# Kernel optimization log

Measured on AMD Instinct MI355X. Metric: run time of the kernel, lower is better.

## Reference

```python
import jax, jax.numpy as jnp
import numpy as np
import math

NUM_HEADS = 32
NUM_KV = 8
D = 128          # num_hidden == per-head dim in this module
S = 2048
B = 1
DK = 128
ROPE_BASE = 10000.0


def rope(x):
    # x: [B, H, S, D]; standard Llama-style RoPE (split-halves rotation) over positions.
    d = x.shape[-1]
    half = d // 2
    pos = jnp.arange(x.shape[2], dtype=jnp.float32)                       # [S]
    inv_freq = 1.0 / (ROPE_BASE ** (jnp.arange(half, dtype=jnp.float32) / half))
    ang = pos[:, None] * inv_freq[None, :]                                # [S, half]
    cos = jnp.cos(ang)
    sin = jnp.sin(ang)
    x1 = x[..., :half]
    x2 = x[..., half:]
    return jnp.concatenate([x1 * cos - x2 * sin, x1 * sin + x2 * cos], axis=-1)


def setup_inputs() -> dict:
    key = jax.random.key(0)
    ks = jax.random.split(key, 8)
    query = jax.random.normal(ks[0], (B, S, D), dtype=jnp.float32)
    k_in = jax.random.normal(ks[1], (B, S, D), dtype=jnp.float32)
    v_in = jax.random.normal(ks[2], (B, S, D), dtype=jnp.float32)
    # causal mask: 1 where attention allowed (lower triangle incl diagonal)
    mask = jnp.tril(jnp.ones((S, S), dtype=jnp.int32))[None, None]        # [1,1,S,S]
    sc = 0.02
    Wq = jax.random.normal(ks[3], (NUM_HEADS * D, D), dtype=jnp.float32) * sc
    bq = jnp.zeros((NUM_HEADS * D,), dtype=jnp.float32)
    Wk = jax.random.normal(ks[4], (NUM_KV * D, D), dtype=jnp.float32) * sc
    bk = jnp.zeros((NUM_KV * D,), dtype=jnp.float32)
    Wv = jax.random.normal(ks[5], (NUM_KV * D, D), dtype=jnp.float32) * sc
    bv = jnp.zeros((NUM_KV * D,), dtype=jnp.float32)
    Wo = jax.random.normal(ks[6], (D, NUM_HEADS * D), dtype=jnp.float32) * sc
    bo = jnp.zeros((D,), dtype=jnp.float32)
    return {"query": query, "key": k_in, "values": v_in, "mask": mask,
            "Wq": Wq, "bq": bq, "Wk": Wk, "bk": bk, "Wv": Wv, "bv": bv,
            "Wo": Wo, "bo": bo}


def reference(query, key, values, mask, Wq, bq, Wk, bk, Wv, bv, Wo, bo):
    Bq, Sq, Dh = query.shape
    # projections; torch Linear: x @ W.T + b. Note: view (reshape), not transpose,
    # exactly as in the original module.
    q = (query @ Wq.T + bq).reshape(Bq, NUM_HEADS, Sq, Dh)   # [B,H,S,D]
    k = (key @ Wk.T + bk).reshape(Bq, NUM_KV, Sq, Dh)        # [B,Hkv,S,D]
    v = (values @ Wv.T + bv).reshape(Bq, NUM_KV, Sq, Dh)
    rk = rope(k)
    rv = rope(v)  # module applies RoPE to values too (faithful)
    rep = NUM_HEADS // NUM_KV
    # torch .repeat((1, rep, 1, 1)) tiles whole head blocks -> jnp.tile
    rk = jnp.tile(rk, (1, rep, 1, 1))                        # [B,H,S,D]
    rv = jnp.tile(rv, (1, rep, 1, 1))
    scores = jnp.einsum('bhqd,bhkd->bhqk', q, rk) / math.sqrt(DK)
    scores = jnp.where(mask == 0, -jnp.inf, scores)
    attn = jax.nn.softmax(scores, axis=-1)
    out = jnp.einsum('bhqk,bhkd->bhqd', attn, rv)            # [B,H,S,D]
    out = out.transpose(0, 2, 1, 3).reshape(Bq, Sq, NUM_HEADS * Dh)
    return out @ Wo.T + bo
```

## Files before the change

### kernel.cpp

```cpp
#include <hip/hip_runtime.h>

typedef unsigned short u16;
typedef unsigned int u32;
typedef short frag_t __attribute__((ext_vector_type(8)));
typedef float f32x4 __attribute__((ext_vector_type(4)));

#define S_LEN 2048

__device__ __forceinline__ float bf2f(u32 u) {
  union { u32 i; float f; } v; v.i = u << 16; return v.f;
}
__device__ __forceinline__ u16 f2bf(float f) {
  u32 x = __float_as_uint(f);
  u32 r = (x + 0x7fffu + ((x >> 16) & 1u)) >> 16;
  return (u16)r;
}
__device__ __forceinline__ void unpack8(uint4 r, float* o) {
  o[0] = bf2f(r.x & 0xffffu); o[1] = bf2f(r.x >> 16);
  o[2] = bf2f(r.y & 0xffffu); o[3] = bf2f(r.y >> 16);
  o[4] = bf2f(r.z & 0xffffu); o[5] = bf2f(r.z >> 16);
  o[6] = bf2f(r.w & 0xffffu); o[7] = bf2f(r.w >> 16);
}
__device__ __forceinline__ u16 ld_in(const void* p, size_t idx, bool fp32) {
  if (fp32) return f2bf(((const float*)p)[idx]);
  return ((const u16*)p)[idx];
}
__device__ __forceinline__ uint4 ld8(const void* p, size_t eidx, bool fp32) {
  if (!fp32) return *(const uint4*)((const u16*)p + eidx);
  const float4* f = (const float4*)((const float*)p + eidx);
  float4 x = f[0], y = f[1];
  uint4 r;
  r.x = (u32)f2bf(x.x) | ((u32)f2bf(x.y) << 16);
  r.y = (u32)f2bf(x.z) | ((u32)f2bf(x.w) << 16);
  r.z = (u32)f2bf(y.x) | ((u32)f2bf(y.y) << 16);
  r.w = (u32)f2bf(y.z) | ((u32)f2bf(y.w) << 16);
  return r;
}

__global__ void detect_dtype(const u16* __restrict__ q, u32* __restrict__ flag) {
  int t = threadIdx.x;
  u32 e = ((u32)q[2 * t] >> 7) & 0xFFu;
  bool ok = (e >= 110u && e <= 140u);
  unsigned long long b = __ballot(ok);
  if (t == 0) *flag = (__popcll(b) < 32) ? 1u : 0u;
}

__global__ __launch_bounds__(256) void proj_all(
    const void* __restrict__ query, const void* __restrict__ key,
    const void* __restrict__ values,
    const void* __restrict__ Wq, const void* __restrict__ bq,
    const void* __restrict__ Wk, const void* __restrict__ bk,
    const void* __restrict__ Wv, const void* __restrict__ bv,
    u16* __restrict__ Qb, u16* __restrict__ Kb, u16* __restrict__ Vtmp,
    const u32* __restrict__ flagp) {
  __shared__ u16 As[64][136];
  __shared__ u16 Ws[64][136];
  const bool fp32 = (*flagp != 0u);
  const int t = threadIdx.x;
  const int x = blockIdx.x;
  const void *A, *W, *bias;
  u16* C; int N, n0;
  if (x < 64)      { A = query;  W = Wq; bias = bq; C = Qb;   N = 4096; n0 = x << 6; }
  else if (x < 80) { A = key;    W = Wk; bias = bk; C = Kb;   N = 1024; n0 = (x - 64) << 6; }
  else             { A = values; W = Wv; bias = bv; C = Vtmp; N = 1024; n0 = (x - 80) << 6; }
  const int m0 = blockIdx.y << 6;
  for (int i = t; i < 1024; i += 256) {
    int r = i >> 4, d8 = (i & 15) << 3;
    *(uint4*)&As[r][d8] = ld8(A, (size_t)(m0 + r) * 128 + d8, fp32);
    *(uint4*)&Ws[r][d8] = ld8(W, (size_t)(n0 + r) * 128 + d8, fp32);
  }
  __syncthreads();
  const int lane = t & 63, w = t >> 6, quad = lane >> 4, l15 = lane & 15;
  f32x4 acc[4];
#pragma unroll
  for (int nt = 0; nt < 4; ++nt) acc[nt] = 0.f;
#pragma unroll
  for (int kc = 0; kc < 4; ++kc) {
    frag_t a = *(const frag_t*)&As[w * 16 + l15][kc * 32 + quad * 8];
#pragma unroll
    for (int nt = 0; nt < 4; ++nt) {
      frag_t b = *(const frag_t*)&Ws[nt * 16 + l15][kc * 32 + quad * 8];
      acc[nt] = __builtin_amdgcn_mfma_f32_16x16x32_bf16(a, b, acc[nt], 0, 0, 0);
    }
  }
#pragma unroll
  for (int nt = 0; nt < 4; ++nt) {
    int n = n0 + nt * 16 + l15;
    float bb = bf2f((u32)ld_in(bias, n, fp32));
#pragma unroll
    for (int r = 0; r < 4; ++r) {
      int m = m0 + w * 16 + quad * 4 + r;
      C[(size_t)m * N + n] = f2bf(acc[nt][r] + bb);
    }
  }
}

__global__ __launch_bounds__(256) void rope_kv_tr(u16* __restrict__ Kb,
                                                  const u16* __restrict__ Vb,
                                                  u16* __restrict__ VbT) {
  __shared__ u16 Lt[128][72];
  const int t = threadIdx.x;
  const int s0 = blockIdx.x << 6;
  const int g = blockIdx.y;
  for (int i = t; i < 4096; i += 256) {
    int s = s0 + (i >> 6), ii = i & 63;
    float invf = __expf(-(float)ii * 0.14391156831212787f);
    float ang = (float)s * invf;
    float sn, cs;
    sincosf(ang, &sn, &cs);
    size_t base = ((size_t)(g << 11) + s) * 128 + ii;
    float k1 = bf2f((u32)Kb[base]), k2 = bf2f((u32)Kb[base + 64]);
    Kb[base] = f2bf(k1 * cs - k2 * sn);
    Kb[base + 64] = f2bf(k1 * sn + k2 * cs);
  }
  const u16* src = Vb + (size_t)g * S_LEN * 128;
  for (int i = t; i < 512; i += 256) {
    int r = i >> 3, d8 = (i & 7) << 3;
    float lo[8], hi[8];
    unpack8(*(const uint4*)&src[(size_t)(s0 + r) * 128 + d8], lo);
    unpack8(*(const uint4*)&src[(size_t)(s0 + r) * 128 + d8 + 64], hi);
#pragma unroll
    for (int j = 0; j < 8; ++j) {
      float invf = __expf(-(float)(d8 + j) * 0.14391156831212787f);
      float ang = (float)(s0 + r) * invf;
      float sn, cs;
      sincosf(ang, &sn, &cs);
      Lt[d8 + j][r] = f2bf(lo[j] * cs - hi[j] * sn);
      Lt[d8 + 64 + j][r] = f2bf(lo[j] * sn + hi[j] * cs);
    }
  }
  __syncthreads();
  u16* dst = VbT + (size_t)g * 128 * S_LEN + s0;
  for (int i = t; i < 2048; i += 256) {
    int d = i >> 4, s4 = (i & 15) << 2;
    uint2 pk;
    pk.x = (u32)Lt[d][s4] | ((u32)Lt[d][s4 + 1] << 16);
    pk.y = (u32)Lt[d][s4 + 2] | ((u32)Lt[d][s4 + 3] << 16);
    *(uint2*)&dst[(size_t)d * S_LEN + s4] = pk;
  }
}

__global__ __launch_bounds__(512, 2) void attn_mfma(
    const u16* __restrict__ Qb, const u16* __restrict__ Kb,
    const u16* __restrict__ VbT, u16* __restrict__ Ob) {
  __shared__ __align__(16) char smem[106496];
  u16 (*Kt)[136] = (u16(*)[136])smem;
  u16 (*Vt)[136] = (u16(*)[136])(smem + 34816);
  u16 (*St)[72]  = (u16(*)[72]) (smem + 69632);
  float* Om = (float*)smem;
  float* Ml = (float*)(smem + 65536);
  const int t = threadIdx.x;
  const int lane = t & 63, w = t >> 6, quad = lane >> 4, l15 = lane & 15;
  const int hw = w & 3, half = w >> 2;
  const int g = blockIdx.y;
  const int pi = blockIdx.x;
  const int h = g + (hw << 3);
  const u16* Kg = Kb + (size_t)g * S_LEN * 128;
  const u16* Vg = VbT + (size_t)g * 128 * S_LEN;
  const int srow = t >> 4, scol = (t & 15) << 3;

  for (int tp = 0; tp < 2; ++tp) {
    const int qt = tp ? pi : 63 - pi;
    const int q0 = qt << 5;
    frag_t aq[2][4];
#pragma unroll
    for (int qp = 0; qp < 2; ++qp)
#pragma unroll
      for (int kc = 0; kc < 4; ++kc)
        aq[qp][kc] = *(const frag_t*)&Qb[((size_t)h * S_LEN + q0 + qp * 16 + l15) * 128 +
                                         kc * 32 + quad * 8];
    float m_r[2] = {-1e30f, -1e30f}, l_r[2] = {0.f, 0.f};
    f32x4 oacc[2][8];
#pragma unroll
    for (int qp = 0; qp < 2; ++qp)
#pragma unroll
      for (int nt = 0; nt < 8; ++nt) oacc[qp][nt] = 0.f;
    const int niter64 = (qt >> 1) + 1;
    const int niter2 = (niter64 + 1) >> 1;

    uint4 kpf[4], vpf[4];
#pragma unroll
    for (int j = 0; j < 4; ++j) {
      kpf[j] = *(const uint4*)&Kg[(size_t)(srow + j * 32) * 128 + scol];
      vpf[j] = *(const uint4*)&Vg[(size_t)(srow + j * 32) * S_LEN + scol];
    }

    for (int kt2 = 0; kt2 < niter2; ++kt2) {
      __syncthreads();
#pragma unroll
      for (int j = 0; j < 4; ++j) {
        *(uint4*)&Kt[srow + j * 32][scol] = kpf[j];
        *(uint4*)&Vt[srow + j * 32][scol] = vpf[j];
      }
      __syncthreads();
      if (kt2 + 1 < niter2) {
        const int kn = (kt2 + 1) << 7;
#pragma unroll
        for (int j = 0; j < 4; ++j) {
          kpf[j] = *(const uint4*)&Kg[(size_t)(kn + srow + j * 32) * 128 + scol];
          vpf[j] = *(const uint4*)&Vg[(size_t)(srow + j * 32) * S_LEN + kn + scol];
        }
      }
      const int tile64 = (kt2 << 1) + half;
      if (tile64 < niter64) {
        const int lk = half << 6;
        const int kbase = (kt2 << 7) + lk;
        f32x4 s4[4][2];
#pragma unroll
        for (int kk = 0; kk < 4; ++kk)
#pragma unroll
          for (int qp = 0; qp < 2; ++qp) s4[kk][qp] = 0.f;
#pragma unroll
        for (int kc = 0; kc < 4; ++kc) {
#pragma unroll
          for (int kk = 0; kk < 4; ++kk) {
            frag_t a = *(const frag_t*)&Kt[lk + kk * 16 + l15][kc * 32 + quad * 8];
            s4[kk][0] = __builtin_amdgcn_mfma_f32_16x16x32_bf16(a, aq[0][kc], s4[kk][0], 0, 0, 0);
            s4[kk][1] = __builtin_amdgcn_mfma_f32_16x16x32_bf16(a, aq[1][kc], s4[kk][1], 0, 0, 0);
          }
        }
        const bool lastm = (tile64 == niter64 - 1);
        float alpha[2];
#pragma unroll
        for (int qp = 0; qp < 2; ++qp) {
          const int qg = q0 + qp * 16 + l15;
          float mx = -1e30f;
#pragma unroll
          for (int kk = 0; kk < 4; ++kk)
#pragma unroll
            for (int r = 0; r < 4; ++r) {
              float sv = s4[kk][qp][r] * 0.08838834764831845f;
              if (lastm && (kbase + kk * 16 + quad * 4 + r) > qg) sv = -1e30f;
              s4[kk][qp][r] = sv;
              mx = fmaxf(mx, sv);
            }
          mx = fmaxf(mx, __shfl_xor(mx, 16));
          mx = fmaxf(mx, __shfl_xor(mx, 32));
          float mn = fmaxf(m_r[qp], mx);
          alpha[qp] = __expf(m_r[qp] - mn);
          m_r[qp] = mn;
          float sum = 0.f;
          const int strow = w * 32 + qp * 16 + l15;
#pragma unroll
          for (int kk = 0; kk < 4; ++kk) {
            float p0 = __expf(s4[kk][qp][0] - mn);
            float p1 = __expf(s4[kk][qp][1] - mn);
            float p2 = __expf(s4[kk][qp][2] - mn);
            float p3 = __expf(s4[kk][qp][3] - mn);
            sum += (p0 + p1) + (p2 + p3);
            uint2 pk;
            pk.x = (u32)f2bf(p0) | ((u32)f2bf(p1) << 16);
            pk.y = (u32)f2bf(p2) | ((u32)f2bf(p3) << 16);
            *(uint2*)&St[strow][kk * 16 + quad * 4] = pk;
          }
          sum += __shfl_xor(sum, 16);
          sum += __shfl_xor(sum, 32);
          l_r[qp] = l_r[qp] * alpha[qp] + sum;
        }
#pragma unroll
        for (int qp = 0; qp < 2; ++qp)
#pragma unroll
          for (int r = 0; r < 4; ++r) {
            float al = __shfl(alpha[qp], quad * 4 + r);
#pragma unroll
            for (int nt = 0; nt < 8; ++nt) oacc[qp][nt][r] *= al;
          }
#pragma unroll
        for (int kc2 = 0; kc2 < 2; ++kc2) {
          frag_t pa[2];
#pragma unroll
          for (int qp = 0; qp < 2; ++qp)
            pa[qp] = *(const frag_t*)&St[w * 32 + qp * 16 + l15][kc2 * 32 + quad * 8];
#pragma unroll
          for (int nt = 0; nt < 8; ++nt) {
            frag_t v = *(const frag_t*)&Vt[nt * 16 + l15][lk + kc2 * 32 + quad * 8];
            oacc[0][nt] = __builtin_amdgcn_mfma_f32_16x16x32_bf16(pa[0], v, oacc[0][nt], 0, 0, 0);
            oacc[1][nt] = __builtin_amdgcn_mfma_f32_16x16x32_bf16(pa[1], v, oacc[1][nt], 0, 0, 0);
          }
        }
      }
    }
    __syncthreads();
    if (half == 1) {
#pragma unroll
      for (int qp = 0; qp < 2; ++qp)
#pragma unroll
        for (int nt = 0; nt < 8; ++nt)
#pragma unroll
          for (int r = 0; r < 4; ++r)
            Om[((hw * 32) + qp * 16 + quad * 4 + r) * 128 + nt * 16 + l15] = oacc[qp][nt][r];
      if (quad == 0) {
#pragma unroll
        for (int qp = 0; qp < 2; ++qp) {
          Ml[hw * 64 + qp * 16 + l15] = m_r[qp];
          Ml[hw * 64 + 32 + qp * 16 + l15] = l_r[qp];
        }
      }
    }
    __syncthreads();
    if (half == 0) {
      float v1[2], v2[2];
#pragma unroll
      for (int qp = 0; qp < 2; ++qp) {
        float m2 = Ml[hw * 64 + qp * 16 + l15];
        float l2 = Ml[hw * 64 + 32 + qp * 16 + l15];
        float mn = fmaxf(m_r[qp], m2);
        float a1 = __expf(m_r[qp] - mn);
        float a2 = __expf(m2 - mn);
        float linv = 1.0f / (a1 * l_r[qp] + a2 * l2);
        v1[qp] = a1 * linv;
        v2[qp] = a2 * linv;
      }
#pragma unroll
      for (int qp = 0; qp < 2; ++qp)
#pragma unroll
        for (int r = 0; r < 4; ++r) {
          float w1 = __shfl(v1[qp], quad * 4 + r);
          float w2 = __shfl(v2[qp], quad * 4 + r);
          int q = q0 + qp * 16 + quad * 4 + r;
#pragma unroll
          for (int nt = 0; nt < 8; ++nt) {
            float o2 = Om[((hw * 32) + qp * 16 + quad * 4 + r) * 128 + nt * 16 + l15];
            Ob[(size_t)q * 4096 + h * 128 + nt * 16 + l15] =
                f2bf(oacc[qp][nt][r] * w1 + o2 * w2);
          }
        }
    }
  }
}

__global__ __launch_bounds__(256) void out_part(
    const u16* __restrict__ Ob, const void* __restrict__ Wo,
    float* __restrict__ Pout, const u32* __restrict__ flagp) {
  __shared__ u16 As[32][72];
  __shared__ u16 Ws[64][72];
  const bool fp32 = (*flagp != 0u);
  const int t = threadIdx.x;
  const int lane = t & 63, w = t >> 6, quad = lane >> 4, l15 = lane & 15;
  const int wm = w & 1, wn = w >> 1;
  const int n0 = (int)blockIdx.x << 6;
  const int m0 = (int)blockIdx.y << 5;
  const int kz = (int)blockIdx.z << 10;
  f32x4 acc[2];
#pragma unroll
  for (int nt = 0; nt < 2; ++nt) acc[nt] = 0.f;
  for (int kc0 = kz; kc0 < kz + 1024; kc0 += 64) {
    if (kc0 != kz) __syncthreads();
    {
      int r = t >> 3, k8 = (t & 7) << 3;
      *(uint4*)&As[r][k8] = *(const uint4*)&Ob[(size_t)(m0 + r) * 4096 + kc0 + k8];
    }
    for (int i = t; i < 512; i += 256) {
      int r = i >> 3, k8 = (i & 7) << 3;
      *(uint4*)&Ws[r][k8] = ld8(Wo, (size_t)(n0 + r) * 4096 + kc0 + k8, fp32);
    }
    __syncthreads();
#pragma unroll
    for (int kc2 = 0; kc2 < 2; ++kc2) {
      frag_t a = *(const frag_t*)&As[wm * 16 + l15][kc2 * 32 + quad * 8];
#pragma unroll
      for (int nt = 0; nt < 2; ++nt) {
        frag_t b = *(const frag_t*)&Ws[wn * 32 + nt * 16 + l15][kc2 * 32 + quad * 8];
        acc[nt] = __builtin_amdgcn_mfma_f32_16x16x32_bf16(a, b, acc[nt], 0, 0, 0);
      }
    }
  }
#pragma unroll
  for (int nt = 0; nt < 2; ++nt) {
    int n = n0 + wn * 32 + nt * 16 + l15;
#pragma unroll
    for (int r = 0; r < 4; ++r) {
      int m = m0 + wm * 16 + quad * 4 + r;
      Pout[((size_t)blockIdx.z * 2048 + m) * 128 + n] = acc[nt][r];
    }
  }
}

__global__ __launch_bounds__(256) void out_red(
    const float* __restrict__ Pout, const void* __restrict__ bo,
    void* __restrict__ out, const u32* __restrict__ flagp) {
  const bool fp32 = (*flagp != 0u);
  int e4 = blockIdx.x * 256 + threadIdx.x;
  const float4* P = (const float4*)Pout;
  float4 s = P[e4];
  float4 s1 = P[65536 + e4], s2 = P[131072 + e4], s3 = P[196608 + e4];
  s.x += s1.x + s2.x + s3.x; s.y += s1.y + s2.y + s3.y;
  s.z += s1.z + s2.z + s3.z; s.w += s1.w + s2.w + s3.w;
  int n = (e4 << 2) & 127;
  s.x += bf2f((u32)ld_in(bo, n + 0, fp32));
  s.y += bf2f((u32)ld_in(bo, n + 1, fp32));
  s.z += bf2f((u32)ld_in(bo, n + 2, fp32));
  s.w += bf2f((u32)ld_in(bo, n + 3, fp32));
  if (fp32) {
    ((float4*)out)[e4] = s;
  } else {
    uint2 pk;
    pk.x = (u32)f2bf(s.x) | ((u32)f2bf(s.y) << 16);
    pk.y = (u32)f2bf(s.z) | ((u32)f2bf(s.w) << 16);
    *(uint2*)((u16*)out + (e4 << 2)) = pk;
  }
}

extern "C" void kernel_launch(void* const* d_in, const int* in_sizes, int n_in,
                              void* d_out, int out_size, void* d_ws, size_t ws_size,
                              hipStream_t stream) {
  (void)in_sizes; (void)n_in; (void)out_size; (void)ws_size;
  const void* query  = d_in[0];
  const void* key    = d_in[1];
  const void* values = d_in[2];
  const void* Wq = d_in[4];
  const void* bq = d_in[5];
  const void* Wk = d_in[6];
  const void* bk = d_in[7];
  const void* Wv = d_in[8];
  const void* bv = d_in[9];
  const void* Wo = d_in[10];
  const void* bo = d_in[11];

  char* ws = (char*)d_ws;
  u32* flag  = (u32*)ws;
  u16* Qb    = (u16*)(ws + 64);
  u16* Kb    = (u16*)(ws + 64 + (16u << 20));
  u16* VbT   = (u16*)(ws + 64 + (20u << 20));
  u16* Vtmp  = (u16*)(ws + 64 + (24u << 20));
  u16* Ob    = (u16*)(ws + 64 + (24u << 20));
  float* Pout = (float*)Qb;

  detect_dtype<<<1, 64, 0, stream>>>((const u16*)query, flag);
  proj_all<<<dim3(96, 32), 256, 0, stream>>>(query, key, values, Wq, bq, Wk, bk,
                                             Wv, bv, Qb, Kb, Vtmp, flag);
  rope_kv_tr<<<dim3(32, 8), 256, 0, stream>>>(Kb, Vtmp, VbT);
  attn_mfma<<<dim3(32, 8), 512, 0, stream>>>(Qb, Kb, VbT, Ob);
  out_part<<<dim3(2, 64, 4), 256, 0, stream>>>(Ob, Wo, Pout, flag);
  out_red<<<256, 256, 0, stream>>>(Pout, bo, d_out, flag);
}
```

Before: 269.6 us.

## Double-buffer 64-key attention tiles and stage output stores through LDS

The attention kernel now processes 64-key super-tiles, with each half of the block taking 32 keys, in place of 128-key tiles. K and V are double-buffered in LDS so that one barrier per iteration suffices and the global loads run two tiles ahead. This halves causal-tail waste, since work is now masked at 32-key granularity. Both the projection and attention epilogues write results to LDS first and then issue coalesced 16-byte global stores instead of scattered 2-byte writes. The cost is more iterations, each with less MFMA work per barrier.

```diff
diff --git a/kernel.cpp b/kernel.cpp
--- a/kernel.cpp
+++ b/kernel.cpp
@@ -55,6 +55,7 @@
     const u32* __restrict__ flagp) {
   __shared__ u16 As[64][136];
   __shared__ u16 Ws[64][136];
+  u16 (*Cs)[72] = (u16(*)[72])&As[0][0];
   const bool fp32 = (*flagp != 0u);
   const int t = threadIdx.x;
   const int x = blockIdx.x;
@@ -83,15 +84,20 @@
       acc[nt] = __builtin_amdgcn_mfma_f32_16x16x32_bf16(a, b, acc[nt], 0, 0, 0);
     }
   }
+  __syncthreads();
 #pragma unroll
   for (int nt = 0; nt < 4; ++nt) {
-    int n = n0 + nt * 16 + l15;
-    float bb = bf2f((u32)ld_in(bias, n, fp32));
-#pragma unroll
-    for (int r = 0; r < 4; ++r) {
-      int m = m0 + w * 16 + quad * 4 + r;
-      C[(size_t)m * N + n] = f2bf(acc[nt][r] + bb);
-    }
+    float bb = bf2f((u32)ld_in(bias, n0 + nt * 16 + l15, fp32));
+#pragma unroll
+    for (int r = 0; r < 4; ++r)
+      Cs[w * 16 + quad * 4 + r][nt * 16 + l15] = f2bf(acc[nt][r] + bb);
+  }
+  __syncthreads();
+#pragma unroll
+  for (int jj = 0; jj < 2; ++jj) {
+    int c = t + (jj << 8);
+    int row = c >> 3, ch = (c & 7) << 3;
+    *(uint4*)&C[(size_t)(m0 + row) * N + n0 + ch] = *(const uint4*)&Cs[row][ch];
   }
 }
 
@@ -143,12 +149,13 @@
 __global__ __launch_bounds__(512, 2) void attn_mfma(
     const u16* __restrict__ Qb, const u16* __restrict__ Kb,
     const u16* __restrict__ VbT, u16* __restrict__ Ob) {
-  __shared__ __align__(16) char smem[106496];
-  u16 (*Kt)[136] = (u16(*)[136])smem;
-  u16 (*Vt)[136] = (u16(*)[136])(smem + 34816);
-  u16 (*St)[72]  = (u16(*)[72]) (smem + 69632);
+  __shared__ __align__(16) char smem[102400];
+  u16 (*Kt)[64][136] = (u16(*)[64][136])smem;
+  u16 (*Vt)[128][72] = (u16(*)[128][72])(smem + 34816);
+  u16 (*St)[40]      = (u16(*)[40])(smem + 71680);
   float* Om = (float*)smem;
   float* Ml = (float*)(smem + 65536);
+  u16 (*Og)[136]     = (u16(*)[136])(smem + 67584);
   const int t = threadIdx.x;
   const int lane = t & 63, w = t >> 6, quad = lane >> 4, l15 = lane & 15;
   const int hw = w & 3, half = w >> 2;
@@ -157,11 +164,14 @@
   const int h = g + (hw << 3);
   const u16* Kg = Kb + (size_t)g * S_LEN * 128;
   const u16* Vg = VbT + (size_t)g * 128 * S_LEN;
-  const int srow = t >> 4, scol = (t & 15) << 3;
+  const int kr0 = t >> 4, kc0 = (t & 15) << 3;
+  const int vr0 = t >> 3, vc0 = (t & 7) << 3;
 
   for (int tp = 0; tp < 2; ++tp) {
     const int qt = tp ? pi : 63 - pi;
     const int q0 = qt << 5;
+    const int niter = qt + 1;
+    const int nsuper = (niter + 1) >> 1;
     frag_t aq[2][4];
 #pragma unroll
     for (int qp = 0; qp < 2; ++qp)
@@ -175,58 +185,70 @@
     for (int qp = 0; qp < 2; ++qp)
 #pragma unroll
       for (int nt = 0; nt < 8; ++nt) oacc[qp][nt] = 0.f;
-    const int niter64 = (qt >> 1) + 1;
-    const int niter2 = (niter64 + 1) >> 1;
-
-    uint4 kpf[4], vpf[4];
-#pragma unroll
-    for (int j = 0; j < 4; ++j) {
-      kpf[j] = *(const uint4*)&Kg[(size_t)(srow + j * 32) * 128 + scol];
-      vpf[j] = *(const uint4*)&Vg[(size_t)(srow + j * 32) * S_LEN + scol];
-    }
-
-    for (int kt2 = 0; kt2 < niter2; ++kt2) {
+
+    uint4 kpf[2], vpf[2];
+#pragma unroll
+    for (int j = 0; j < 2; ++j) {
+      kpf[j] = *(const uint4*)&Kg[(size_t)(kr0 + j * 32) * 128 + kc0];
+      vpf[j] = *(const uint4*)&Vg[(size_t)(vr0 + j * 64) * S_LEN + vc0];
+    }
+#pragma unroll
+    for (int j = 0; j < 2; ++j) {
+      *(uint4*)&Kt[0][kr0 + j * 32][kc0] = kpf[j];
+      *(uint4*)&Vt[0][vr0 + j * 64][vc0] = vpf[j];
+    }
+    if (nsuper > 1) {
+#pragma unroll
+      for (int j = 0; j < 2; ++j) {
+        kpf[j] = *(const uint4*)&Kg[(size_t)(64 + kr0 + j * 32) * 128 + kc0];
+        vpf[j] = *(const uint4*)&Vg[(size_t)(vr0 + j * 64) * S_LEN + 64 + vc0];
+      }
+    }
+
+    for (int sj = 0; sj < nsuper; ++sj) {
       __syncthreads();
-#pragma unroll
-      for (int j = 0; j < 4; ++j) {
-        *(uint4*)&Kt[srow + j * 32][scol] = kpf[j];
-        *(uint4*)&Vt[srow + j * 32][scol] = vpf[j];
-      }
-      __syncthreads();
-      if (kt2 + 1 < niter2) {
-        const int kn = (kt2 + 1) << 7;
-#pragma unroll
-        for (int j = 0; j < 4; ++j) {
-          kpf[j] = *(const uint4*)&Kg[(size_t)(kn + srow + j * 32) * 128 + scol];
-          vpf[j] = *(const uint4*)&Vg[(size_t)(srow + j * 32) * S_LEN + kn + scol];
-        }
-      }
-      const int tile64 = (kt2 << 1) + half;
-      if (tile64 < niter64) {
-        const int lk = half << 6;
-        const int kbase = (kt2 << 7) + lk;
-        f32x4 s4[4][2];
-#pragma unroll
-        for (int kk = 0; kk < 4; ++kk)
+      const int buf = sj & 1;
+      if (sj + 1 < nsuper) {
+#pragma unroll
+        for (int j = 0; j < 2; ++j) {
+          *(uint4*)&Kt[buf ^ 1][kr0 + j * 32][kc0] = kpf[j];
+          *(uint4*)&Vt[buf ^ 1][vr0 + j * 64][vc0] = vpf[j];
+        }
+      }
+      if (sj + 2 < nsuper) {
+        const int kn = (sj + 2) << 6;
+#pragma unroll
+        for (int j = 0; j < 2; ++j) {
+          kpf[j] = *(const uint4*)&Kg[(size_t)(kn + kr0 + j * 32) * 128 + kc0];
+          vpf[j] = *(const uint4*)&Vg[(size_t)(vr0 + j * 64) * S_LEN + kn + vc0];
+        }
+      }
+      const int tile32 = (sj << 1) + half;
+      if (tile32 < niter) {
+        const int kbase = tile32 << 5;
+        const int lk = half << 5;
+        f32x4 s4[2][2];
+#pragma unroll
+        for (int kk = 0; kk < 2; ++kk)
 #pragma unroll
           for (int qp = 0; qp < 2; ++qp) s4[kk][qp] = 0.f;
 #pragma unroll
         for (int kc = 0; kc < 4; ++kc) {
 #pragma unroll
-          for (int kk = 0; kk < 4; ++kk) {
-            frag_t a = *(const frag_t*)&Kt[lk + kk * 16 + l15][kc * 32 + quad * 8];
+          for (int kk = 0; kk < 2; ++kk) {
+            frag_t a = *(const frag_t*)&Kt[buf][lk + kk * 16 + l15][kc * 32 + quad * 8];
             s4[kk][0] = __builtin_amdgcn_mfma_f32_16x16x32_bf16(a, aq[0][kc], s4[kk][0], 0, 0, 0);
             s4[kk][1] = __builtin_amdgcn_mfma_f32_16x16x32_bf16(a, aq[1][kc], s4[kk][1], 0, 0, 0);
           }
         }
-        const bool lastm = (tile64 == niter64 - 1);
+        const bool lastm = (tile32 == niter - 1);
         float alpha[2];
 #pragma unroll
         for (int qp = 0; qp < 2; ++qp) {
           const int qg = q0 + qp * 16 + l15;
           float mx = -1e30f;
 #pragma unroll
-          for (int kk = 0; kk < 4; ++kk)
+          for (int kk = 0; kk < 2; ++kk)
 #pragma unroll
             for (int r = 0; r < 4; ++r) {
               float sv = s4[kk][qp][r] * 0.08838834764831845f;
@@ -242,7 +264,7 @@
           float sum = 0.f;
           const int strow = w * 32 + qp * 16 + l15;
 #pragma unroll
-          for (int kk = 0; kk < 4; ++kk) {
+          for (int kk = 0; kk < 2; ++kk) {
             float p0 = __expf(s4[kk][qp][0] - mn);
             float p1 = __expf(s4[kk][qp][1] - mn);
             float p2 = __expf(s4[kk][qp][2] - mn);
@@ -265,18 +287,15 @@
 #pragma unroll
             for (int nt = 0; nt < 8; ++nt) oacc[qp][nt][r] *= al;
           }
-#pragma unroll
-        for (int kc2 = 0; kc2 < 2; ++kc2) {
-          frag_t pa[2];
-#pragma unroll
-          for (int qp = 0; qp < 2; ++qp)
-            pa[qp] = *(const frag_t*)&St[w * 32 + qp * 16 + l15][kc2 * 32 + quad * 8];
-#pragma unroll
-          for (int nt = 0; nt < 8; ++nt) {
-            frag_t v = *(const frag_t*)&Vt[nt * 16 + l15][lk + kc2 * 32 + quad * 8];
-            oacc[0][nt] = __builtin_amdgcn_mfma_f32_16x16x32_bf16(pa[0], v, oacc[0][nt], 0, 0, 0);
-            oacc[1][nt] = __builtin_amdgcn_mfma_f32_16x16x32_bf16(pa[1], v, oacc[1][nt], 0, 0, 0);
-          }
+        frag_t pa[2];
+#pragma unroll
+        for (int qp = 0; qp < 2; ++qp)
+          pa[qp] = *(const frag_t*)&St[w * 32 + qp * 16 + l15][quad * 8];
+#pragma unroll
+        for (int nt = 0; nt < 8; ++nt) {
+          frag_t v = *(const frag_t*)&Vt[buf][nt * 16 + l15][lk + quad * 8];
+          oacc[0][nt] = __builtin_amdgcn_mfma_f32_16x16x32_bf16(pa[0], v, oacc[0][nt], 0, 0, 0);
+          oacc[1][nt] = __builtin_amdgcn_mfma_f32_16x16x32_bf16(pa[1], v, oacc[1][nt], 0, 0, 0);
         }
       }
     }
@@ -317,14 +336,22 @@
         for (int r = 0; r < 4; ++r) {
           float w1 = __shfl(v1[qp], quad * 4 + r);
           float w2 = __shfl(v2[qp], quad * 4 + r);
-          int q = q0 + qp * 16 + quad * 4 + r;
 #pragma unroll
           for (int nt = 0; nt < 8; ++nt) {
             float o2 = Om[((hw * 32) + qp * 16 + quad * 4 + r) * 128 + nt * 16 + l15];
-            Ob[(size_t)q * 4096 + h * 128 + nt * 16 + l15] =
+            Og[hw * 32 + qp * 16 + quad * 4 + r][nt * 16 + l15] =
                 f2bf(oacc[qp][nt][r] * w1 + o2 * w2);
           }
         }
+    }
+    __syncthreads();
+#pragma unroll
+    for (int jj = 0; jj < 4; ++jj) {
+      int c = t + (jj << 9);
+      int row = c >> 4, ch = (c & 15) << 3;
+      int hh = row >> 5, qr = row & 31;
+      *(uint4*)&Ob[(size_t)(q0 + qr) * 4096 + (g + hh * 8) * 128 + ch] =
+          *(const uint4*)&Og[row][ch];
     }
   }
 }
```

After: 257.8 us. -4.4%, faster.
